# Performance work log

Measured on AMD Instinct MI355X. Metric: run time of the kernel, lower is better.

Reference implementation:

```python
import jax, jax.numpy as jnp
import numpy as np

N_NODES = 100000
N_EDGES = 1600000
IN_DIM = 128
HID = 64
OUT = 64


def setup_inputs() -> dict:
    key = jax.random.key(0)
    ks = jax.random.split(key, 8)
    feats = jax.random.normal(ks[0], (N_NODES, IN_DIM), dtype=jnp.float32)
    src = jax.random.randint(ks[1], (N_EDGES,), 0, N_NODES)
    dst = jax.random.randint(ks[2], (N_EDGES,), 0, N_NODES)
    W1 = jax.random.normal(ks[3], (IN_DIM, HID), dtype=jnp.float32) * (1.0 / np.sqrt(IN_DIM))
    b1 = jnp.zeros((HID,), jnp.float32)
    W2 = jax.random.normal(ks[4], (HID, HID), dtype=jnp.float32) * (1.0 / np.sqrt(HID))
    b2 = jnp.zeros((HID,), jnp.float32)
    Wout = jax.random.normal(ks[5], (2 * HID, OUT), dtype=jnp.float32) * (1.0 / np.sqrt(2 * HID))
    bout = jnp.zeros((OUT,), jnp.float32)
    return {"feats": feats, "src": src, "dst": dst, "W1": W1, "b1": b1,
            "W2": W2, "b2": b2, "Wout": Wout, "bout": bout}


def reference(feats, src, dst, W1, b1, W2, b2, Wout, bout):
    N = feats.shape[0]
    ones = jnp.ones(src.shape[0], dtype=feats.dtype)
    # DGL GraphConv norm='both': symmetric degree normalization, degrees clamped to >= 1
    deg_out = jnp.maximum(jax.ops.segment_sum(ones, src, num_segments=N), 1.0)
    deg_in = jnp.maximum(jax.ops.segment_sum(ones, dst, num_segments=N), 1.0)
    norm_s = deg_out ** -0.5  # [N]
    norm_d = deg_in ** -0.5   # [N]

    def gconv(x, W, b):
        h = (x * norm_s[:, None]) @ W                      # transform (order-equivalent)
        agg = jax.ops.segment_sum(h[src], dst, num_segments=N)  # sparse neighbor sum
        return jax.nn.relu(agg * norm_d[:, None] + b)

    h1 = gconv(feats, W1, b1)   # [N, HID]
    h2 = gconv(h1, W2, b2)      # [N, HID]
    jumped = jnp.concatenate([h1, h2], axis=-1)  # JK 'cat' -> [N, 2*HID]
    # Concate module: unnormalized copy_u/sum aggregation
    agged = jax.ops.segment_sum(jumped[src], dst, num_segments=N)
    return agged @ Wout + bout
```

## Files before the change

### kernel.cpp

```cpp
#include <hip/hip_runtime.h>

static inline int divup(long a, long b){ return (int)((a + b - 1) / b); }

typedef float f32x4 __attribute__((ext_vector_type(4)));

#define CAP    64
#define BSHIFT 9
#define BNODES 512
#define CAP_E  12288
#define PBLK   256


__global__ void k_zero32(unsigned* __restrict__ p, long n){
  long i = (long)blockIdx.x * blockDim.x + threadIdx.x;
  long st = (long)gridDim.x * blockDim.x;
  for (; i < n; i += st) p[i] = 0u;
}

__global__ __launch_bounds__(256) void k_part2(const int* __restrict__ src,
    const int* __restrict__ dst, int E, int per,
    int* __restrict__ curD, int* __restrict__ curS,
    unsigned* __restrict__ partD, int* __restrict__ partS)
{
  __shared__ int hD[256], hS[256];
  const int t = threadIdx.x;
  const int b0 = blockIdx.x * per, b1 = min(E, b0 + per);
  hD[t] = 0; hS[t] = 0;
  __syncthreads();
  for (int i = b0 + t; i < b1; i += 256){
    atomicAdd(&hD[dst[i] >> BSHIFT], 1);
    atomicAdd(&hS[src[i] >> BSHIFT], 1);
  }
  __syncthreads();
  { int c = hD[t]; hD[t] = c ? atomicAdd(&curD[t], c) : 0;
    c = hS[t];     hS[t] = c ? atomicAdd(&curS[t], c) : 0; }
  __syncthreads();
  for (int i = b0 + t; i < b1; i += 256){
    int s = src[i], d = dst[i];
    int bD = d >> BSHIFT;
    int p = atomicAdd(&hD[bD], 1);
    if (p < CAP_E)
      partD[(long)bD * CAP_E + p] = ((unsigned)(d & (BNODES - 1)) << 17) | (unsigned)s;
    int bS = s >> BSHIFT;
    int q = atomicAdd(&hS[bS], 1);
    if (q < CAP_E)
      partS[(long)bS * CAP_E + q] = s;
  }
}

__global__ __launch_bounds__(256) void k_csr_degs(const int* __restrict__ curD,
    const int* __restrict__ curS, unsigned* __restrict__ partD,
    const int* __restrict__ partS, int* __restrict__ rowptr,
    int* __restrict__ degD, int* __restrict__ degS, int N)
{
  __shared__ unsigned ed[CAP_E];
  __shared__ int cnt[BNODES], scn[BNODES], tmp[256];
  const int B = blockIdx.x, t = threadIdx.x;
  const long base = (long)B * CAP_E;
  int m = curD[B]; if (m > CAP_E) m = CAP_E;
  for (int i = t; i < BNODES; i += 256) cnt[i] = 0;
  __syncthreads();
  for (int i = t; i < m; i += 256){
    unsigned p = partD[base + i];
    ed[i] = p;
    atomicAdd(&cnt[p >> 17], 1);
  }
  __syncthreads();
  int a0 = cnt[2 * t], a1 = cnt[2 * t + 1];
  int s = a0 + a1;
  tmp[t] = s;
  __syncthreads();
  for (int off = 1; off < 256; off <<= 1){
    int v = (t >= off) ? tmp[t - off] : 0;
    __syncthreads();
    tmp[t] += v;
    __syncthreads();
  }
  int excl = tmp[t] - s;
  scn[2 * t]     = excl;
  scn[2 * t + 1] = excl + a0;
  __syncthreads();
  const int nodeBase = B << BSHIFT;
  for (int i = t; i < BNODES; i += 256){
    int node = nodeBase + i;
    if (node < N){ rowptr[node] = (int)base + scn[i]; degD[node] = cnt[i]; }
  }
  __syncthreads();
  int* csr = (int*)partD;
  for (int i = t; i < m; i += 256){
    unsigned p = ed[i];
    int slot = atomicAdd(&scn[p >> 17], 1);
    csr[base + slot] = (int)(p & 0x1FFFFu);
  }
  int mS = curS[B]; if (mS > CAP_E) mS = CAP_E;
  __syncthreads();
  for (int i = t; i < BNODES; i += 256) cnt[i] = 0;
  __syncthreads();
  for (int i = t; i < mS; i += 256)
    atomicAdd(&cnt[partS[base + i] & (BNODES - 1)], 1);
  __syncthreads();
  for (int i = t; i < BNODES; i += 256){
    int node = nodeBase + i;
    if (node < N) degS[node] = cnt[i];
  }
}

template<int MODE>
__global__ __launch_bounds__(256) void k_agg(const float* __restrict__ h,
    const int* __restrict__ rowptr, const int* __restrict__ degD,
    const int* __restrict__ csr, const float* __restrict__ bias,
    float* __restrict__ out, int N)
{
  int node = blockIdx.x * 4 + (threadIdx.x >> 6);
  if (node >= N) return;
  int lane = threadIdx.x & 63;
  int eg = lane >> 4;
  int c4 = (lane & 15) << 2;
  int beg = rowptr[node];
  int deg = degD[node];
  int end = beg + deg;

  float ax = 0.f, ay = 0.f, az = 0.f, aw = 0.f;
  float bx = 0.f, by = 0.f, bz = 0.f, bw = 0.f;
  int p = beg + eg;
  for (; p + 12 < end; p += 16){
    int s0 = __builtin_nontemporal_load(csr + p);
    int s1 = __builtin_nontemporal_load(csr + p + 4);
    int s2 = __builtin_nontemporal_load(csr + p + 8);
    int s3 = __builtin_nontemporal_load(csr + p + 12);
    float4 v0 = *(const float4*)&h[(long)s0 * 64 + c4];
    float4 v1 = *(const float4*)&h[(long)s1 * 64 + c4];
    float4 v2 = *(const float4*)&h[(long)s2 * 64 + c4];
    float4 v3 = *(const float4*)&h[(long)s3 * 64 + c4];
    ax += v0.x; ay += v0.y; az += v0.z; aw += v0.w;
    bx += v1.x; by += v1.y; bz += v1.z; bw += v1.w;
    ax += v2.x; ay += v2.y; az += v2.z; aw += v2.w;
    bx += v3.x; by += v3.y; bz += v3.z; bw += v3.w;
  }
  for (; p < end; p += 4){
    int s = __builtin_nontemporal_load(csr + p);
    float4 v = *(const float4*)&h[(long)s * 64 + c4];
    ax += v.x; ay += v.y; az += v.z; aw += v.w;
  }
  ax += bx; ay += by; az += bz; aw += bw;

  ax += __shfl_xor(ax, 16); ay += __shfl_xor(ay, 16);
  az += __shfl_xor(az, 16); aw += __shfl_xor(aw, 16);
  ax += __shfl_xor(ax, 32); ay += __shfl_xor(ay, 32);
  az += __shfl_xor(az, 32); aw += __shfl_xor(aw, 32);

  if (eg == 0){
    float4 bb = *(const float4*)&bias[c4];
    f32x4 r;
    if constexpr (MODE == 1){
      float nd = rsqrtf((float)(deg < 1 ? 1 : deg));
      r.x = fmaxf(fmaf(ax, nd, bb.x), 0.f);
      r.y = fmaxf(fmaf(ay, nd, bb.y), 0.f);
      r.z = fmaxf(fmaf(az, nd, bb.z), 0.f);
      r.w = fmaxf(fmaf(aw, nd, bb.w), 0.f);
    } else {
      r.x = ax + bb.x; r.y = ay + bb.y; r.z = az + bb.z; r.w = aw + bb.w;
    }
    __builtin_nontemporal_store(r, (f32x4*)&out[(long)node * 64 + c4]);
  }
}

template<int K0, int K1, bool SCALE>
__global__ __launch_bounds__(256) void k_gemm(
    const float* __restrict__ A0, const float* __restrict__ A1,
    const float* __restrict__ W, const int* __restrict__ degS,
    float* __restrict__ out, int N)
{
  constexpr int K   = K0 + K1;
  constexpr int KD4 = K / 4;
  constexpr int LDA = K + 4;
  __shared__ float sA[128 * LDA];
  __shared__ float sW[K * 64];
  const int tid  = threadIdx.x;
  const int brow = blockIdx.x * 128;

  for (int idx = tid; idx < K * 16; idx += 256){
    int k  = idx >> 4;
    int c4 = (idx & 15) << 2;
    *(float4*)&sW[k * 64 + c4] = *(const float4*)&W[k * 64 + c4];
  }
  for (int idx = tid; idx < 128 * KD4; idx += 256){
    int r  = idx / KD4;
    int kk = idx - r * KD4;
    int k  = kk << 2;
    int row = brow + r;
    float4 v = make_float4(0.f, 0.f, 0.f, 0.f);
    if (row < N){
      if constexpr (K1 == 0){
        v = *(const float4*)&A0[(long)row * K0 + k];
      } else {
        if (k < K0) v = *(const float4*)&A0[(long)row * K0 + k];
        else        v = *(const float4*)&A1[(long)row * K1 + (k - K0)];
      }
      if constexpr (SCALE){
        int dg = degS[row];
        float s = rsqrtf((float)(dg < 1 ? 1 : dg));
        v.x *= s; v.y *= s; v.z *= s; v.w *= s;
      }
    }
    *(float4*)&sA[r * LDA + k] = v;
  }
  __syncthreads();

  const int tx = tid & 15, ty = tid >> 4;
  const int c0 = tx << 2;
  float4 acc[8];
  #pragma unroll
  for (int i = 0; i < 8; i++) acc[i] = make_float4(0.f, 0.f, 0.f, 0.f);

  const float4* sW4 = (const float4*)sW;
  #pragma unroll 2
  for (int kk = 0; kk < KD4; ++kk){
    float4 w0 = sW4[(4 * kk + 0) * 16 + tx];
    float4 w1 = sW4[(4 * kk + 1) * 16 + tx];
    float4 w2 = sW4[(4 * kk + 2) * 16 + tx];
    float4 w3 = sW4[(4 * kk + 3) * 16 + tx];
    #pragma unroll
    for (int i = 0; i < 8; i++){
      float4 a = *(const float4*)&sA[(ty + 16 * i) * LDA + (kk << 2)];
      acc[i].x += a.x * w0.x + a.y * w1.x + a.z * w2.x + a.w * w3.x;
      acc[i].y += a.x * w0.y + a.y * w1.y + a.z * w2.y + a.w * w3.y;
      acc[i].z += a.x * w0.z + a.y * w1.z + a.z * w2.z + a.w * w3.z;
      acc[i].w += a.x * w0.w + a.y * w1.w + a.z * w2.w + a.w * w3.w;
    }
  }
  #pragma unroll
  for (int i = 0; i < 8; i++){
    int row = brow + ty + 16 * i;
    if (row < N) *(float4*)&out[(long)row * 64 + c0] = acc[i];
  }
}


__global__ void k_prep(const int* __restrict__ src, const int* __restrict__ dst,
                       int* __restrict__ degS, int* __restrict__ degD,
                       int* __restrict__ padded, int E){
  int i = blockIdx.x * blockDim.x + threadIdx.x;
  if (i >= E) return;
  int s = src[i], d = dst[i];
  int slot = atomicAdd(&degD[d], 1);
  if (slot < CAP) padded[(long)d * CAP + slot] = s;
  atomicAdd(&degS[s], 1);
}

template<int MODE>
__global__ __launch_bounds__(256) void k_agg_pad(const float* __restrict__ h,
    const int* __restrict__ padded, const int* __restrict__ degD,
    const float* __restrict__ bias, float* __restrict__ out, int N)
{
  int node = blockIdx.x * 4 + (threadIdx.x >> 6);
  if (node >= N) return;
  int lane = threadIdx.x & 63;
  int deg = degD[node];
  int len = deg < CAP ? deg : CAP;
  const int* row = padded + (long)node * CAP;
  int sid = (lane < len) ? row[lane] : 0;
  float acc0 = 0.f, acc1 = 0.f;
  int t = 0;
  for (; t + 4 <= len; t += 4){
    int s0 = __shfl(sid, t),   s1 = __shfl(sid, t+1);
    int s2 = __shfl(sid, t+2), s3 = __shfl(sid, t+3);
    acc0 += h[(long)s0 * 64 + lane];
    acc1 += h[(long)s1 * 64 + lane];
    acc0 += h[(long)s2 * 64 + lane];
    acc1 += h[(long)s3 * 64 + lane];
  }
  for (; t < len; ++t){
    int s = __shfl(sid, t);
    acc0 += h[(long)s * 64 + lane];
  }
  float acc = acc0 + acc1;
  float r;
  if constexpr (MODE == 1){
    float nd = rsqrtf((float)(deg < 1 ? 1 : deg));
    r = fmaxf(fmaf(acc, nd, bias[lane]), 0.f);
  } else {
    r = acc + bias[lane];
  }
  out[(long)node * 64 + lane] = r;
}


extern "C" void kernel_launch(void* const* d_in, const int* in_sizes, int n_in,
                              void* d_out, int out_size, void* d_ws, size_t ws_size,
                              hipStream_t stream){
  const float* feats = (const float*)d_in[0];
  const int*   src   = (const int*)  d_in[1];
  const int*   dst   = (const int*)  d_in[2];
  const float* W1    = (const float*)d_in[3];
  const float* b1    = (const float*)d_in[4];
  const float* W2    = (const float*)d_in[5];
  const float* b2    = (const float*)d_in[6];
  const float* Wout  = (const float*)d_in[7];
  const float* bout  = (const float*)d_in[8];
  float* out = (float*)d_out;

  const int N = in_sizes[0] / 128;
  const int E = in_sizes[1];

  const int gemmGrid = divup(N, 128);
  const int aggGrid  = divup(N, 4);
  const int nb       = divup(N, BNODES);

  size_t needA = ((size_t)(3L * N) + 512
                + 2L * (size_t)nb * CAP_E
                + 192L * N) * 4;
  if (N <= 131072 && nb <= 256 && ws_size >= needA){
    int*      degS   = (int*)d_ws;
    int*      degD   = degS + N;
    int*      rowptr = degD + N;
    int*      curD   = rowptr + N;
    int*      curS   = curD + 256;
    unsigned* partD  = (unsigned*)(curS + 256);
    int*      partS  = (int*)(partD + (long)nb * CAP_E);
    float*    ht     = (float*)(partS + (long)nb * CAP_E);
    float*    h1     = ht + 64L * N;
    float*    h2     = h1 + 64L * N;
    int*      csr    = (int*)partD;

    k_zero32<<<1, 256, 0, stream>>>((unsigned*)curD, 512);
    k_part2<<<PBLK, 256, 0, stream>>>(src, dst, E, divup(E, PBLK), curD, curS, partD, partS);
    k_csr_degs<<<nb, 256, 0, stream>>>(curD, curS, partD, partS, rowptr, degD, degS, N);

    k_gemm<128, 0, true><<<gemmGrid, 256, 0, stream>>>(feats, nullptr, W1, degS, ht, N);
    k_agg<1><<<aggGrid, 256, 0, stream>>>(ht, rowptr, degD, csr, b1, h1, N);

    k_gemm<64, 0, true><<<gemmGrid, 256, 0, stream>>>(h1, nullptr, W2, degS, ht, N);
    k_agg<1><<<aggGrid, 256, 0, stream>>>(ht, rowptr, degD, csr, b2, h2, N);

    k_gemm<64, 64, false><<<gemmGrid, 256, 0, stream>>>(h1, h2, Wout, nullptr, ht, N);
    k_agg<0><<<aggGrid, 256, 0, stream>>>(ht, rowptr, degD, csr, bout, out, N);
    return;
  }

  int*   degS   = (int*)d_ws;
  int*   degD   = degS + N;
  int*   padded = degD + N;
  float* ht     = (float*)(padded + (long)CAP * N);
  float* h1     = ht + 64L * N;
  float* h2     = h1 + 64L * N;

  k_zero32<<<256, 256, 0, stream>>>((unsigned*)degS, 2L * N);
  k_prep<<<divup(E, 256), 256, 0, stream>>>(src, dst, degS, degD, padded, E);

  k_gemm<128, 0, true><<<gemmGrid, 256, 0, stream>>>(feats, nullptr, W1, degS, ht, N);
  k_agg_pad<1><<<aggGrid, 256, 0, stream>>>(ht, padded, degD, b1, h1, N);

  k_gemm<64, 0, true><<<gemmGrid, 256, 0, stream>>>(h1, nullptr, W2, degS, ht, N);
  k_agg_pad<1><<<aggGrid, 256, 0, stream>>>(ht, padded, degD, b2, h2, N);

  k_gemm<64, 64, false><<<gemmGrid, 256, 0, stream>>>(h1, h2, Wout, nullptr, ht, N);
  k_agg_pad<0><<<aggGrid, 256, 0, stream>>>(ht, padded, degD, bout, out, N);
}
```

Before: 417.2 us.

## Rework dense GEMM to 256-row tiles with K-chunked shared memory staging

The GEMM kernel now processes 256 rows per block and loops over K in 32-wide chunks, staging only one chunk of A and W in shared memory at a time. Each thread computes 8 rows by 8 columns instead of 8 rows by 4, which raises register-level reuse of the loaded A and W values. The smaller shared memory footprint is meant to allow more blocks per CU for the K=128 case. The cost is extra syncthreads per chunk, more registers per thread, and half as many blocks in the grid.

```diff
diff --git a/kernel.cpp b/kernel.cpp
--- a/kernel.cpp
+++ b/kernel.cpp
@@ -172,67 +172,80 @@
     float* __restrict__ out, int N)
 {
   constexpr int K   = K0 + K1;
-  constexpr int KD4 = K / 4;
-  constexpr int LDA = K + 4;
-  __shared__ float sA[128 * LDA];
-  __shared__ float sW[K * 64];
+  constexpr int NCH = K / 32;
+  __shared__ float sA[256 * 36];
+  __shared__ float sW[32 * 64];
   const int tid  = threadIdx.x;
-  const int brow = blockIdx.x * 128;
-
-  for (int idx = tid; idx < K * 16; idx += 256){
-    int k  = idx >> 4;
-    int c4 = (idx & 15) << 2;
-    *(float4*)&sW[k * 64 + c4] = *(const float4*)&W[k * 64 + c4];
-  }
-  for (int idx = tid; idx < 128 * KD4; idx += 256){
-    int r  = idx / KD4;
-    int kk = idx - r * KD4;
-    int k  = kk << 2;
-    int row = brow + r;
-    float4 v = make_float4(0.f, 0.f, 0.f, 0.f);
-    if (row < N){
-      if constexpr (K1 == 0){
-        v = *(const float4*)&A0[(long)row * K0 + k];
-      } else {
-        if (k < K0) v = *(const float4*)&A0[(long)row * K0 + k];
-        else        v = *(const float4*)&A1[(long)row * K1 + (k - K0)];
-      }
-      if constexpr (SCALE){
-        int dg = degS[row];
-        float s = rsqrtf((float)(dg < 1 ? 1 : dg));
-        v.x *= s; v.y *= s; v.z *= s; v.w *= s;
-      }
-    }
-    *(float4*)&sA[r * LDA + k] = v;
-  }
-  __syncthreads();
-
-  const int tx = tid & 15, ty = tid >> 4;
-  const int c0 = tx << 2;
-  float4 acc[8];
-  #pragma unroll
-  for (int i = 0; i < 8; i++) acc[i] = make_float4(0.f, 0.f, 0.f, 0.f);
-
-  const float4* sW4 = (const float4*)sW;
-  #pragma unroll 2
-  for (int kk = 0; kk < KD4; ++kk){
-    float4 w0 = sW4[(4 * kk + 0) * 16 + tx];
-    float4 w1 = sW4[(4 * kk + 1) * 16 + tx];
-    float4 w2 = sW4[(4 * kk + 2) * 16 + tx];
-    float4 w3 = sW4[(4 * kk + 3) * 16 + tx];
-    #pragma unroll
-    for (int i = 0; i < 8; i++){
-      float4 a = *(const float4*)&sA[(ty + 16 * i) * LDA + (kk << 2)];
-      acc[i].x += a.x * w0.x + a.y * w1.x + a.z * w2.x + a.w * w3.x;
-      acc[i].y += a.x * w0.y + a.y * w1.y + a.z * w2.y + a.w * w3.y;
-      acc[i].z += a.x * w0.z + a.y * w1.z + a.z * w2.z + a.w * w3.z;
-      acc[i].w += a.x * w0.w + a.y * w1.w + a.z * w2.w + a.w * w3.w;
-    }
-  }
+  const int brow = blockIdx.x * 256;
+  const int tx = tid & 7, ty = tid >> 3;
+
+  float4 acc[8][2];
   #pragma unroll
   for (int i = 0; i < 8; i++){
-    int row = brow + ty + 16 * i;
-    if (row < N) *(float4*)&out[(long)row * 64 + c0] = acc[i];
+    acc[i][0] = make_float4(0.f, 0.f, 0.f, 0.f);
+    acc[i][1] = make_float4(0.f, 0.f, 0.f, 0.f);
+  }
+
+  for (int ch = 0; ch < NCH; ++ch){
+    if (ch) __syncthreads();
+    #pragma unroll
+    for (int it = 0; it < 2; it++){
+      int id = tid + it * 256;
+      int k = id >> 4, c4 = (id & 15) << 2;
+      *(float4*)&sW[k * 64 + c4] = *(const float4*)&W[(ch * 32 + k) * 64 + c4];
+    }
+    #pragma unroll
+    for (int it = 0; it < 8; it++){
+      int id = tid + it * 256;
+      int r = id >> 3, kk = id & 7;
+      int row = brow + r;
+      int k = ch * 32 + kk * 4;
+      float4 v = make_float4(0.f, 0.f, 0.f, 0.f);
+      if (row < N){
+        if constexpr (K1 == 0){
+          v = *(const float4*)&A0[(long)row * K0 + k];
+        } else {
+          if (k < K0) v = *(const float4*)&A0[(long)row * K0 + k];
+          else        v = *(const float4*)&A1[(long)row * K1 + (k - K0)];
+        }
+        if constexpr (SCALE){
+          int dg = degS[row];
+          float s = rsqrtf((float)(dg < 1 ? 1 : dg));
+          v.x *= s; v.y *= s; v.z *= s; v.w *= s;
+        }
+      }
+      *(float4*)&sA[r * 36 + kk * 4] = v;
+    }
+    __syncthreads();
+    #pragma unroll
+    for (int kk = 0; kk < 8; kk++){
+      float4 w0[4], w1[4];
+      #pragma unroll
+      for (int k4 = 0; k4 < 4; k4++){
+        w0[k4] = *(const float4*)&sW[(kk * 4 + k4) * 64 + tx * 8];
+        w1[k4] = *(const float4*)&sW[(kk * 4 + k4) * 64 + tx * 8 + 4];
+      }
+      #pragma unroll
+      for (int i = 0; i < 8; i++){
+        float4 a = *(const float4*)&sA[(ty + 32 * i) * 36 + kk * 4];
+        acc[i][0].x += a.x*w0[0].x + a.y*w0[1].x + a.z*w0[2].x + a.w*w0[3].x;
+        acc[i][0].y += a.x*w0[0].y + a.y*w0[1].y + a.z*w0[2].y + a.w*w0[3].y;
+        acc[i][0].z += a.x*w0[0].z + a.y*w0[1].z + a.z*w0[2].z + a.w*w0[3].z;
+        acc[i][0].w += a.x*w0[0].w + a.y*w0[1].w + a.z*w0[2].w + a.w*w0[3].w;
+        acc[i][1].x += a.x*w1[0].x + a.y*w1[1].x + a.z*w1[2].x + a.w*w1[3].x;
+        acc[i][1].y += a.x*w1[0].y + a.y*w1[1].y + a.z*w1[2].y + a.w*w1[3].y;
+        acc[i][1].z += a.x*w1[0].z + a.y*w1[1].z + a.z*w1[2].z + a.w*w1[3].z;
+        acc[i][1].w += a.x*w1[0].w + a.y*w1[1].w + a.z*w1[2].w + a.w*w1[3].w;
+      }
+    }
+  }
+  #pragma unroll
+  for (int i = 0; i < 8; i++){
+    int row = brow + ty + 32 * i;
+    if (row < N){
+      *(float4*)&out[(long)row * 64 + tx * 8]     = acc[i][0];
+      *(float4*)&out[(long)row * 64 + tx * 8 + 4] = acc[i][1];
+    }
   }
 }
 
@@ -303,7 +316,7 @@
   const int N = in_sizes[0] / 128;
   const int E = in_sizes[1];
 
-  const int gemmGrid = divup(N, 128);
+  const int gemmGrid = divup(N, 256);
   const int aggGrid  = divup(N, 4);
   const int nb       = divup(N, BNODES);
 
```

Result: slower. 445.2 us (+6.7%).
